# Kernel optimization log

Measured on AMD Instinct MI355X. Metric: run time of the kernel, lower is better.

Reference implementation:

```python
import jax, jax.numpy as jnp
import numpy as np

N_ENTITY, N_REL, DIM, H = 500000, 32, 64, 2
N_ITEM, N_MEM, BATCH, HIST = 10000, 32, 4096, 50


def setup_inputs() -> dict:
    key = jax.random.key(0)
    ks = jax.random.split(key, 10)
    return {
        "entity_emb": jax.random.normal(ks[0], (N_ENTITY, DIM), jnp.float32) * 0.05,
        "relation_emb": jax.random.normal(ks[1], (N_REL, DIM), jnp.float32) * 0.05,
        "W_w": jax.random.normal(ks[2], (1, 3 * DIM), jnp.float32) * 0.05,
        "W_b": jnp.zeros((1,), jnp.float32),
        "item_ids": jax.random.randint(ks[3], (N_ITEM,), 0, N_ENTITY, jnp.int32),
        "heads": jax.random.randint(ks[4], (H, N_ITEM, N_MEM), 0, N_ENTITY, jnp.int32),
        "relations": jax.random.randint(ks[5], (H, N_ITEM, N_MEM), 0, N_REL, jnp.int32),
        "tails": jax.random.randint(ks[6], (H, N_ITEM, N_MEM), 0, N_ENTITY, jnp.int32),
        "records_idx": jax.random.randint(ks[7], (BATCH, HIST), 0, N_ITEM, jnp.int32),
        "items": jax.random.randint(ks[8], (BATCH,), 0, N_ENTITY, jnp.int32),
    }


def reference(entity_emb, relation_emb, W_w, W_b, item_ids, heads, relations, tails, records_idx, items):
    d = entity_emb.shape[1]
    # Split the Linear(3d->1) weight so we never materialize the [n_item,m,3d] concat.
    w_h, w_r, w_t = W_w[0, :d], W_w[0, d:2 * d], W_w[0, 2 * d:]
    # Hop-0 item embedding (base entity embedding of each candidate item).
    acc = entity_emb[item_ids]  # [n_item, d]
    for h in range(heads.shape[0]):
        te = entity_emb[tails[h]]  # [n_item, m, d]
        logits = (entity_emb[heads[h]] @ w_h
                  + relation_emb[relations[h]] @ w_r
                  + te @ w_t + W_b[0])  # [n_item, m]
        # Original: sigmoid then softmax over the memory axis.
        pi = jax.nn.softmax(jax.nn.sigmoid(logits), axis=1)[..., None]
        acc = acc + (pi * te).sum(axis=1)
    # User embedding = sum of (hop-enhanced) item embeddings over history records.
    user_emb = acc[records_idx].sum(axis=1)  # [B, d]
    pair_item = entity_emb[items]            # [B, d] (raw entity embedding)
    return jax.nn.sigmoid(jnp.sum(user_emb * pair_item, axis=-1))
```

## Files before the change

kernel.cpp:

```cpp
#include <hip/hip_runtime.h>
#include <math.h>

#define DIM    64
#define N_MEM  32
#define N_ITEM 10000
#define HOPS   2
#define BATCH  4096
#define HIST   50

typedef float4 f4;


__global__ __launch_bounds__(256) void ripple_stage1(
    const float* __restrict__ entity_emb,
    const float* __restrict__ relation_emb,
    const float* __restrict__ W_w,
    const float* __restrict__ W_b,
    const int*   __restrict__ item_ids,
    const int*   __restrict__ heads,
    const int*   __restrict__ relations,
    const int*   __restrict__ tails,
    float*       __restrict__ acc_out)
{
    const int wave = (blockIdx.x * blockDim.x + threadIdx.x) >> 6;
    const int lane = threadIdx.x & 63;
    if (wave >= N_ITEM) return;
    const int g = lane >> 4;
    const int p = lane & 15;

    const f4* __restrict__ E4 = (const f4*)entity_emb;
    const f4* __restrict__ R4 = (const f4*)relation_emb;
    const f4* __restrict__ W4 = (const f4*)W_w;

    const f4 wh = W4[p];
    const f4 wr = W4[16 + p];
    const f4 wt = W4[32 + p];
    const float bias = W_b[0];

    f4 acc = {0.f, 0.f, 0.f, 0.f};
    {
        const f4 it = E4[(size_t)item_ids[wave] * 16 + p];
        if (g == 0) acc = it;
    }

#pragma unroll
    for (int h = 0; h < HOPS; ++h) {
        const int base = (h * N_ITEM + wave) * N_MEM + g;

        f4    te[8];
        float part[8];
#pragma unroll
        for (int k = 0; k < 8; ++k) {
            const int hi = heads[base + 4 * k];
            const int ri = relations[base + 4 * k];
            const int ti = tails[base + 4 * k];
            const f4 he = E4[(size_t)hi * 16 + p];
            const f4 re = R4[(size_t)ri * 16 + p];
            const f4 t  = E4[(size_t)ti * 16 + p];
            te[k] = t;
            part[k] = he.x * wh.x + he.y * wh.y + he.z * wh.z + he.w * wh.w
                    + re.x * wr.x + re.y * wr.y + re.z * wr.z + re.w * wr.w
                    + t.x  * wt.x + t.y  * wt.y + t.z  * wt.z + t.w  * wt.w;
        }

        float e[8];
        float se = 0.f;
#pragma unroll
        for (int k = 0; k < 8; ++k) {
            float v = part[k];
            v += __shfl_xor(v, 1, 64);
            v += __shfl_xor(v, 2, 64);
            v += __shfl_xor(v, 4, 64);
            v += __shfl_xor(v, 8, 64);
            const float logit = v + bias;
            const float sig   = 1.f / (1.f + __expf(-logit));
            const float ex    = __expf(sig);
            e[k] = ex;
            se += ex;
        }
        se += __shfl_xor(se, 16, 64);
        se += __shfl_xor(se, 32, 64);
        const float inv = 1.f / se;

#pragma unroll
        for (int k = 0; k < 8; ++k) {
            const float w = e[k] * inv;
            acc.x += w * te[k].x;
            acc.y += w * te[k].y;
            acc.z += w * te[k].z;
            acc.w += w * te[k].w;
        }
    }

    acc.x += __shfl_xor(acc.x, 16, 64);
    acc.x += __shfl_xor(acc.x, 32, 64);
    acc.y += __shfl_xor(acc.y, 16, 64);
    acc.y += __shfl_xor(acc.y, 32, 64);
    acc.z += __shfl_xor(acc.z, 16, 64);
    acc.z += __shfl_xor(acc.z, 32, 64);
    acc.w += __shfl_xor(acc.w, 16, 64);
    acc.w += __shfl_xor(acc.w, 32, 64);
    if (g == 0) ((f4*)acc_out)[(size_t)wave * 16 + p] = acc;
}

__global__ __launch_bounds__(256) void ripple_stage2(
    const float* __restrict__ entity_emb,
    const int*   __restrict__ records_idx,
    const int*   __restrict__ items,
    const float* __restrict__ acc_buf,
    float*       __restrict__ out)
{
    const int wave = (blockIdx.x * blockDim.x + threadIdx.x) >> 6;
    const int lane = threadIdx.x & 63;
    if (wave >= BATCH) return;
    const int b = wave;
    const int g = lane >> 4;
    const int p = lane & 15;

    const f4* __restrict__ A4 = (const f4*)acc_buf;
    const f4* __restrict__ E4 = (const f4*)entity_emb;

    f4 user = {0.f, 0.f, 0.f, 0.f};
    const int rb = b * HIST;
#pragma unroll
    for (int k = 0; k < 13; ++k) {
        const int j  = 4 * k + g;
        const int jc = j < HIST ? j : (HIST - 1);
        const float w = j < HIST ? 1.f : 0.f;
        const int idx = records_idx[rb + jc];
        const f4 r = A4[(size_t)idx * 16 + p];
        user.x += w * r.x;
        user.y += w * r.y;
        user.z += w * r.z;
        user.w += w * r.w;
    }
    user.x += __shfl_xor(user.x, 16, 64);
    user.x += __shfl_xor(user.x, 32, 64);
    user.y += __shfl_xor(user.y, 16, 64);
    user.y += __shfl_xor(user.y, 32, 64);
    user.z += __shfl_xor(user.z, 16, 64);
    user.z += __shfl_xor(user.z, 32, 64);
    user.w += __shfl_xor(user.w, 16, 64);
    user.w += __shfl_xor(user.w, 32, 64);

    const f4 pair = E4[(size_t)items[b] * 16 + p];
    float dot = user.x * pair.x + user.y * pair.y + user.z * pair.z + user.w * pair.w;
    dot += __shfl_xor(dot, 1, 64);
    dot += __shfl_xor(dot, 2, 64);
    dot += __shfl_xor(dot, 4, 64);
    dot += __shfl_xor(dot, 8, 64);
    if (lane == 0) out[b] = 1.f / (1.f + __expf(-dot));
}

extern "C" void kernel_launch(void* const* d_in, const int* in_sizes, int n_in,
                              void* d_out, int out_size, void* d_ws, size_t ws_size,
                              hipStream_t stream) {
    const float* entity_emb   = (const float*)d_in[0];
    const float* relation_emb = (const float*)d_in[1];
    const float* W_w          = (const float*)d_in[2];
    const float* W_b          = (const float*)d_in[3];
    const int*   item_ids     = (const int*)d_in[4];
    const int*   heads        = (const int*)d_in[5];
    const int*   relations    = (const int*)d_in[6];
    const int*   tails        = (const int*)d_in[7];
    const int*   records_idx  = (const int*)d_in[8];
    const int*   items        = (const int*)d_in[9];
    float* out = (float*)d_out;

    float* acc_buf = (float*)d_ws;

    const int blocks1 = (N_ITEM + 3) / 4;
    ripple_stage1<<<blocks1, 256, 0, stream>>>(entity_emb, relation_emb, W_w, W_b,
                                               item_ids, heads, relations, tails,
                                               acc_buf);

    const int blocks2 = (BATCH + 3) / 4;
    ripple_stage2<<<blocks2, 256, 0, stream>>>(entity_emb, records_idx, items,
                                               acc_buf, out);
}
```

Measured before the change: 229.5 us.

## Split hops across waves and batch gather loads ahead of compute

Stage 1 now launches one wave per (hop, item) pair instead of one per item, which doubles the number of waves so more random gathers are in flight. All index loads and then all embedding gathers are issued before any arithmetic. Each hop writes its partial result to its own slot in an interleaved [item][hop] workspace, and stage 2 reads both slots and adds them. This costs twice the workspace writes, extra gathers in stage 2 and more registers per thread in exchange for more memory-level parallelism.

New measurement: 230.0 us. No clear change (+0.2%).

```diff
diff --git a/kernel.cpp b/kernel.cpp
--- a/kernel.cpp
+++ b/kernel.cpp
@@ -24,7 +24,9 @@
 {
     const int wave = (blockIdx.x * blockDim.x + threadIdx.x) >> 6;
     const int lane = threadIdx.x & 63;
-    if (wave >= N_ITEM) return;
+    if (wave >= HOPS * N_ITEM) return;
+    const int h = wave < N_ITEM ? 0 : 1;
+    const int i = wave - h * N_ITEM;
     const int g = lane >> 4;
     const int p = lane & 15;
 
@@ -37,59 +39,63 @@
     const f4 wt = W4[32 + p];
     const float bias = W_b[0];
 
-    f4 acc = {0.f, 0.f, 0.f, 0.f};
-    {
-        const f4 it = E4[(size_t)item_ids[wave] * 16 + p];
-        if (g == 0) acc = it;
+    const int base = wave * N_MEM + g;
+
+    int hi[8], ri[8], ti[8];
+#pragma unroll
+    for (int k = 0; k < 8; ++k) {
+        hi[k] = heads[base + 4 * k];
+        ri[k] = relations[base + 4 * k];
+        ti[k] = tails[base + 4 * k];
     }
 
+    f4 he[8], re[8], te[8];
 #pragma unroll
-    for (int h = 0; h < HOPS; ++h) {
-        const int base = (h * N_ITEM + wave) * N_MEM + g;
+    for (int k = 0; k < 8; ++k) he[k] = E4[(size_t)hi[k] * 16 + p];
+#pragma unroll
+    for (int k = 0; k < 8; ++k) re[k] = R4[(size_t)ri[k] * 16 + p];
+#pragma unroll
+    for (int k = 0; k < 8; ++k) te[k] = E4[(size_t)ti[k] * 16 + p];
 
-        f4    te[8];
-        float part[8];
+    f4 acc = {0.f, 0.f, 0.f, 0.f};
+    if (h == 0) {
+        if (g == 0) acc = E4[(size_t)item_ids[i] * 16 + p];
+    }
+
+    float part[8];
 #pragma unroll
-        for (int k = 0; k < 8; ++k) {
-            const int hi = heads[base + 4 * k];
-            const int ri = relations[base + 4 * k];
-            const int ti = tails[base + 4 * k];
-            const f4 he = E4[(size_t)hi * 16 + p];
-            const f4 re = R4[(size_t)ri * 16 + p];
-            const f4 t  = E4[(size_t)ti * 16 + p];
-            te[k] = t;
-            part[k] = he.x * wh.x + he.y * wh.y + he.z * wh.z + he.w * wh.w
-                    + re.x * wr.x + re.y * wr.y + re.z * wr.z + re.w * wr.w
-                    + t.x  * wt.x + t.y  * wt.y + t.z  * wt.z + t.w  * wt.w;
-        }
+    for (int k = 0; k < 8; ++k) {
+        part[k] = he[k].x * wh.x + he[k].y * wh.y + he[k].z * wh.z + he[k].w * wh.w
+                + re[k].x * wr.x + re[k].y * wr.y + re[k].z * wr.z + re[k].w * wr.w
+                + te[k].x * wt.x + te[k].y * wt.y + te[k].z * wt.z + te[k].w * wt.w;
+    }
 
-        float e[8];
-        float se = 0.f;
+    float e[8];
+    float se = 0.f;
 #pragma unroll
-        for (int k = 0; k < 8; ++k) {
-            float v = part[k];
-            v += __shfl_xor(v, 1, 64);
-            v += __shfl_xor(v, 2, 64);
-            v += __shfl_xor(v, 4, 64);
-            v += __shfl_xor(v, 8, 64);
-            const float logit = v + bias;
-            const float sig   = 1.f / (1.f + __expf(-logit));
-            const float ex    = __expf(sig);
-            e[k] = ex;
-            se += ex;
-        }
-        se += __shfl_xor(se, 16, 64);
-        se += __shfl_xor(se, 32, 64);
-        const float inv = 1.f / se;
+    for (int k = 0; k < 8; ++k) {
+        float v = part[k];
+        v += __shfl_xor(v, 1, 64);
+        v += __shfl_xor(v, 2, 64);
+        v += __shfl_xor(v, 4, 64);
+        v += __shfl_xor(v, 8, 64);
+        const float logit = v + bias;
+        const float sig   = 1.f / (1.f + __expf(-logit));
+        const float ex    = __expf(sig);
+        e[k] = ex;
+        se += ex;
+    }
+    se += __shfl_xor(se, 16, 64);
+    se += __shfl_xor(se, 32, 64);
+    const float inv = 1.f / se;
 
 #pragma unroll
-        for (int k = 0; k < 8; ++k) {
-            const float w = e[k] * inv;
-            acc.x += w * te[k].x;
-            acc.y += w * te[k].y;
-            acc.z += w * te[k].z;
-            acc.w += w * te[k].w;
-        }
+    for (int k = 0; k < 8; ++k) {
+        const float w = e[k] * inv;
+        acc.x += w * te[k].x;
+        acc.y += w * te[k].y;
+        acc.z += w * te[k].z;
+        acc.w += w * te[k].w;
     }
 
     acc.x += __shfl_xor(acc.x, 16, 64);
@@ -100,7 +106,7 @@
     acc.z += __shfl_xor(acc.z, 32, 64);
     acc.w += __shfl_xor(acc.w, 16, 64);
     acc.w += __shfl_xor(acc.w, 32, 64);
-    if (g == 0) ((f4*)acc_out)[(size_t)wave * 16 + p] = acc;
+    if (g == 0) ((f4*)acc_out)[((size_t)i * 2 + h) * 16 + p] = acc;
 }
 
 __global__ __launch_bounds__(256) void ripple_stage2(
@@ -120,19 +126,27 @@
     const f4* __restrict__ A4 = (const f4*)acc_buf;
     const f4* __restrict__ E4 = (const f4*)entity_emb;
 
-    f4 user = {0.f, 0.f, 0.f, 0.f};
     const int rb = b * HIST;
+    int idx[13];
+    float wgt[13];
 #pragma unroll
     for (int k = 0; k < 13; ++k) {
         const int j  = 4 * k + g;
         const int jc = j < HIST ? j : (HIST - 1);
-        const float w = j < HIST ? 1.f : 0.f;
-        const int idx = records_idx[rb + jc];
-        const f4 r = A4[(size_t)idx * 16 + p];
-        user.x += w * r.x;
-        user.y += w * r.y;
-        user.z += w * r.z;
-        user.w += w * r.w;
+        wgt[k] = j < HIST ? 1.f : 0.f;
+        idx[k] = records_idx[rb + jc];
+    }
+
+    f4 user = {0.f, 0.f, 0.f, 0.f};
+#pragma unroll
+    for (int k = 0; k < 13; ++k) {
+        const size_t r = (size_t)idx[k] * 32 + p;
+        const f4 r0 = A4[r];
+        const f4 r1 = A4[r + 16];
+        user.x += wgt[k] * (r0.x + r1.x);
+        user.y += wgt[k] * (r0.y + r1.y);
+        user.z += wgt[k] * (r0.z + r1.z);
+        user.w += wgt[k] * (r0.w + r1.w);
     }
     user.x += __shfl_xor(user.x, 16, 64);
     user.x += __shfl_xor(user.x, 32, 64);
@@ -169,7 +183,8 @@
 
     float* acc_buf = (float*)d_ws;
 
-    const int blocks1 = (N_ITEM + 3) / 4;
+    const int waves1  = HOPS * N_ITEM;
+    const int blocks1 = (waves1 + 3) / 4;
     ripple_stage1<<<blocks1, 256, 0, stream>>>(entity_emb, relation_emb, W_w, W_b,
                                                item_ids, heads, relations, tails,
                                                acc_buf);
```
